# Performance work log

Hardware: AMD Instinct MI355X
Metric: run time of the kernel (lower is better)

The kernel has to match this reference:

```python
import jax, jax.numpy as jnp
import numpy as np

WSZ = 8
HEADS = 8
FILTER_RATE = 0.3
EPS = 1e-5


def layer_norm(x, w, b):
    mu = x.mean(-1, keepdims=True)
    var = ((x - mu) ** 2).mean(-1, keepdims=True)
    return (x - mu) * jax.lax.rsqrt(var + EPS) * w + b


def setup_inputs() -> dict:
    key = jax.random.key(0)
    ks = jax.random.split(key, 8)
    B, C, H, W = 2, 256, 512, 512
    C2 = 2 * C
    s = 0.02
    return {
        "feature_map": jax.random.normal(ks[0], (B, C, H, W), jnp.float32),
        "uncertain_map": jax.random.uniform(ks[1], (B, H, W), jnp.float32),
        "norm_w": jnp.ones((C,), jnp.float32),
        "norm_b": jnp.zeros((C,), jnp.float32),
        "lin0_w": jax.random.normal(ks[2], (C, C2), jnp.float32) * s,
        "lin0_b": jnp.zeros((C2,), jnp.float32),
        "qkv0_w": jax.random.normal(ks[3], (C2, 3 * C2), jnp.float32) * s,
        "lin1_w": jax.random.normal(ks[4], (C2, C2), jnp.float32) * s,
        "lin1_b": jnp.zeros((C2,), jnp.float32),
        "qkv1_w": jax.random.normal(ks[5], (C2, 3 * C2), jnp.float32) * s,
        "proj_w": jax.random.normal(ks[6], (C2, C), jnp.float32) * s,
        "proj_b": jnp.zeros((C,), jnp.float32),
    }


def _window_attn(xf, qkv_w, scale, winsz, C2):
    # xf: (N, winsz, C2)
    qkv = (xf @ qkv_w).reshape(-1, winsz, 3, HEADS, C2 // HEADS)
    q, k, v = qkv[:, :, 0], qkv[:, :, 1], qkv[:, :, 2]  # (N, winsz, H, dh)
    a = jnp.einsum("nqhd,nkhd->nhqk", q, k) * scale
    a = jax.nn.softmax(a, axis=-1)
    o = jnp.einsum("nhqk,nkhd->nqhd", a, v).reshape(-1, winsz, C2)
    return xf + o


def reference(feature_map, uncertain_map, norm_w, norm_b, lin0_w, lin0_b,
              qkv0_w, lin1_w, lin1_b, qkv1_w, proj_w, proj_b):
    B, C, H, W = feature_map.shape
    wsz = WSZ
    nH, nW = H // wsz, W // wsz
    nWin, winsz = nH * nW, wsz * wsz
    nWF = int(nWin * FILTER_RATE)
    C2 = 2 * C
    scale = (C // HEADS) ** -0.5  # module uses C//num_heads, not C2//num_heads

    # window partition
    x = jnp.transpose(feature_map, (0, 2, 3, 1))  # B H W C
    win_x = x.reshape(B, nH, wsz, nW, wsz, C).transpose(0, 1, 3, 2, 4, 5)
    win_x = win_x.reshape(B * nWin, winsz, C)
    win_unc = uncertain_map.reshape(B, nH, wsz, nW, wsz).transpose(0, 1, 3, 2, 4)
    win_unc = win_unc.reshape(B, nWin, winsz)

    # topk window selection by mean uncertainty
    score = win_unc.mean(-1)  # (B, nWin)
    _, idx = jax.lax.top_k(score, nWF)  # (B, nWF)
    flat_idx = (idx + jnp.arange(B)[:, None] * nWin).reshape(-1)  # (B*nWF,)

    xw = win_x[flat_idx]  # gather: (B*nWF, winsz, C)
    xn = layer_norm(xw, norm_w, norm_b)

    # local branch: repeat 0
    xf = jax.nn.gelu(xn @ lin0_w + lin0_b, approximate=False)
    xf = _window_attn(xf, qkv0_w, scale, winsz, C2)
    # repeat 1
    xf = xf + jax.nn.gelu(xf @ lin1_w + lin1_b, approximate=False)
    xf = _window_attn(xf, qkv1_w, scale, winsz, C2)

    out_f = xn + jax.nn.gelu(xf @ proj_w + proj_b, approximate=False)

    # scatter-add back into unnormalized windows
    win_x = win_x.at[flat_idx].add(out_f)

    x = win_x.reshape(B, nH, nW, wsz, wsz, C).transpose(0, 1, 3, 2, 4, 5)
    x = x.reshape(B, H, W, C)
    return jnp.transpose(x, (0, 3, 1, 2))
```

## Files before the change

kernel.cpp:

```cpp
#include <hip/hip_runtime.h>
#include <math.h>

typedef unsigned short u16;
typedef unsigned int   u32;
typedef __attribute__((ext_vector_type(8))) short bf16x8;
typedef __attribute__((ext_vector_type(4))) float f32x4;

#define DEV static __device__ __forceinline__

DEV u16 f2b(float f) {
  union { float f; u32 u; } v; v.f = f;
  u32 r = v.u + 0x7FFFu + ((v.u >> 16) & 1u);
  return (u16)(r >> 16);
}
DEV float b2f(u16 h) {
  union { u32 u; float f; } v; v.u = ((u32)h) << 16;
  return v.f;
}
DEV float gelu_f(float x) { return 0.5f * x * (1.0f + erff(x * 0.70710678118654752f)); }

DEV void gload16(const u16* g, u16* l) {
  __builtin_amdgcn_global_load_lds(
      (const __attribute__((address_space(1))) void*)g,
      (__attribute__((address_space(3))) void*)l, 16, 0, 0);
}

__global__ void k_transpose_w(const float* __restrict__ src, u16* __restrict__ dst,
                              int K, int N) {
  long t = (long)blockIdx.x * 256 + threadIdx.x;
  if (t >= (long)K * N) return;
  int n = (int)(t / K), k = (int)(t % K);
  dst[t] = f2b(src[(long)k * N + n]);
}

__global__ void k_scores(const float* __restrict__ unc, float* __restrict__ scores) {
  int id = blockIdx.x * 256 + threadIdx.x;
  if (id >= 8192) return;
  int b = id >> 12, win = id & 4095;
  int h0 = (win >> 6) << 3, w0 = (win & 63) << 3;
  float r[8] = {0.f,0.f,0.f,0.f,0.f,0.f,0.f,0.f};
  for (int i = 0; i < 8; ++i) {
    long base = ((long)(b * 512 + h0 + i)) * 512 + w0;
    #pragma unroll
    for (int j = 0; j < 8; ++j) r[j] += unc[base + j];
  }
  float s = ((r[0] + r[1]) + (r[2] + r[3])) + ((r[4] + r[5]) + (r[6] + r[7]));
  scores[id] = s * (1.0f / 64.0f);
}

__global__ __launch_bounds__(1024) void k_topk(
    const float* __restrict__ scores, int* __restrict__ row2win,
    int* __restrict__ win2row, int nWF) {
  __shared__ float ls[4096];
  __shared__ int   li[4096];
  const int b = blockIdx.x;
  const int tid = threadIdx.x;
  for (int i = tid; i < 4096; i += 1024) {
    ls[i] = scores[b * 4096 + i];
    li[i] = i;
    win2row[b * 4096 + i] = -1;
  }
  __syncthreads();
  for (int k = 2; k <= 4096; k <<= 1) {
    for (int j = k >> 1; j > 0; j >>= 1) {
      for (int t = tid; t < 2048; t += 1024) {
        int i = ((t / j) * (j << 1)) + (t % j);
        int ixj = i + j;
        bool up = ((i & k) == 0);
        float sa = ls[i], sb = ls[ixj];
        int ia = li[i], ib = li[ixj];
        bool g = (sa > sb) || (sa == sb && ia < ib);
        if (g != up) { ls[i] = sb; ls[ixj] = sa; li[i] = ib; li[ixj] = ia; }
      }
      __syncthreads();
    }
  }
  for (int r = tid; r < nWF; r += 1024) {
    int win = li[r];
    row2win[b * nWF + r] = (b << 12) | win;
    win2row[b * 4096 + win] = b * nWF + r;
  }
}

__global__ __launch_bounds__(256) void k_gather_ln(
    const float* __restrict__ fm, const float* __restrict__ nw,
    const float* __restrict__ nb, const int* __restrict__ row2win,
    u16* __restrict__ xn, int winStart) {
  __shared__ float sx[64 * 256];
  const int tid = threadIdx.x;
  const int rw = row2win[winStart + blockIdx.x];
  const int b = rw >> 12, win = rw & 4095;
  const int h0 = (win >> 6) << 3, w0 = (win & 63) << 3;
  {
    const int c8 = tid >> 3, h = tid & 7;
    #pragma unroll
    for (int cc = 0; cc < 8; ++cc) {
      const int c = cc * 32 + c8;
      long base = ((long)(b * 256 + c) * 512 + h0 + h) * 512 + w0;
      float4 v0 = *(const float4*)(fm + base);
      float4 v1 = *(const float4*)(fm + base + 4);
      float vv[8] = {v0.x, v0.y, v0.z, v0.w, v1.x, v1.y, v1.z, v1.w};
      #pragma unroll
      for (int j = 0; j < 8; ++j) {
        int tok = h * 8 + j;
        sx[tok * 256 + (c ^ ((tok & 15) << 1))] = vv[j];
      }
    }
  }
  __syncthreads();
  const int tok = tid >> 2, g = tid & 3;
  const int swz = (tok & 15) << 1;
  float sum = 0.f;
  for (int q = 0; q < 64; ++q) sum += sx[tok * 256 + ((g * 64 + q) ^ swz)];
  sum += __shfl_xor(sum, 1);
  sum += __shfl_xor(sum, 2);
  const float mu = sum * (1.0f / 256.0f);
  float s2 = 0.f;
  for (int q = 0; q < 64; ++q) {
    float d = sx[tok * 256 + ((g * 64 + q) ^ swz)] - mu;
    s2 += d * d;
  }
  s2 += __shfl_xor(s2, 1);
  s2 += __shfl_xor(s2, 2);
  const float rs = rsqrtf(s2 * (1.0f / 256.0f) + 1e-5f);
  long obase = ((long)blockIdx.x * 64 + tok) * 256 + g * 64;
  for (int q8 = 0; q8 < 8; ++q8) {
    u16 tmp[8];
    #pragma unroll
    for (int e = 0; e < 8; ++e) {
      int c = g * 64 + q8 * 8 + e;
      float v = (sx[tok * 256 + (c ^ swz)] - mu) * rs * nw[c] + nb[c];
      tmp[e] = f2b(v);
    }
    *(ulonglong2*)(xn + obase + q8 * 8) = *(const ulonglong2*)tmp;
  }
}

template <int EPI, int NT, int KD>
__global__ __launch_bounds__(512, 2) void k_gemm256(
    const u16* __restrict__ A, const u16* __restrict__ Bt,
    const float* __restrict__ bias, const u16* __restrict__ Res,
    u16* __restrict__ Y, int N) {
  __shared__ __attribute__((aligned(16))) u16 S[65536];
  const int tid = threadIdx.x;
  const int l = tid & 63, wid = tid >> 6;
  const int wm = wid >> 2, wn = wid & 3;

  const int nwg = gridDim.x;
  const int d = blockIdx.x;
  const int xcd = d & 7, j = d >> 3;
  const int q = nwg >> 3, r8 = nwg & 7;
  const int wrk = (xcd < r8 ? xcd * (q + 1) : r8 * (q + 1) + (xcd - r8) * q) + j;
  const int tm = wrk / NT, tn = wrk % NT;

  const int srow = wid * 8 + (l >> 3);
  const int k0b = ((l & 7) << 4) ^ ((l >> 3) << 4);
  const u16* gA = A + (long)(tm * 256 + srow) * KD + (k0b >> 1);
  const u16* gB = Bt + (long)(tn * 256 + srow) * KD + (k0b >> 1);
  char* ldsS = (char*)S + wid * 1024 + l * 16;
  const char* Sb = (const char*)S;

  f32x4 acc[8][4] = {};
  bf16x8 bfrag[4][2];
  bf16x8 af[2][2];

#define STG(T, ISB, H) do { \
    const u16* g_ = (ISB) ? gB : gA; \
    char* lp_ = ldsS + ((T) & 1) * 65536 + (ISB) * 32768 + (H) * 16384; \
    gload16(g_ + (long)((H) * 128) * KD + (long)(T) * 64, (u16*)lp_); \
    gload16(g_ + (long)((H) * 128 + 64) * KD + (long)(T) * 64, (u16*)(lp_ + 8192)); \
  } while (0)

#define DS_B(T) do { \
    _Pragma("unroll") for (int ni_ = 0; ni_ < 4; ++ni_) { \
      const int r_ = wn * 64 + ni_ * 16 + (l & 15); \
      _Pragma("unroll") for (int kk_ = 0; kk_ < 2; ++kk_) { \
        const int kb_ = kk_ * 64 + ((l >> 4) << 4); \
        bfrag[ni_][kk_] = *(const bf16x8*)(Sb + ((T) & 1) * 65536 + 32768 + r_ * 128 + (kb_ ^ ((r_ & 7) << 4))); \
      } } \
  } while (0)

#define DS_A(T, Q) do { \
    _Pragma("unroll") for (int m2_ = 0; m2_ < 2; ++m2_) { \
      const int r_ = wm * 128 + (2 * (Q) + m2_) * 16 + (l & 15); \
      _Pragma("unroll") for (int kk_ = 0; kk_ < 2; ++kk_) { \
        const int kb_ = kk_ * 64 + ((l >> 4) << 4); \
        af[m2_][kk_] = *(const bf16x8*)(Sb + ((T) & 1) * 65536 + r_ * 128 + (kb_ ^ ((r_ & 7) << 4))); \
      } } \
  } while (0)

#define MFMA16(Q) do { \
    _Pragma("unroll") for (int m2_ = 0; m2_ < 2; ++m2_) \
      _Pragma("unroll") for (int ni_ = 0; ni_ < 4; ++ni_) \
        _Pragma("unroll") for (int kk_ = 0; kk_ < 2; ++kk_) \
          acc[2 * (Q) + m2_][ni_] = __builtin_amdgcn_mfma_f32_16x16x32_bf16( \
              af[m2_][kk_], bfrag[ni_][kk_], acc[2 * (Q) + m2_][ni_], 0, 0, 0); \
  } while (0)

#define BAR_MFMA(Q) do { \
    __builtin_amdgcn_s_barrier(); \
    asm volatile("s_waitcnt lgkmcnt(0)" ::: "memory"); \
    __builtin_amdgcn_sched_barrier(0); \
    __builtin_amdgcn_s_setprio(1); \
    MFMA16(Q); \
    __builtin_amdgcn_s_setprio(0); \
  } while (0)

#define PH_END() do { \
    __builtin_amdgcn_s_barrier(); \
    __builtin_amdgcn_sched_barrier(0); \
  } while (0)

  STG(0, 0, 0); STG(0, 0, 1); STG(0, 1, 0); STG(0, 1, 1);
  STG(1, 0, 0); STG(1, 0, 1); STG(1, 1, 0); STG(1, 1, 1);
  asm volatile("s_waitcnt vmcnt(8)" ::: "memory");
  __builtin_amdgcn_s_barrier();
  __builtin_amdgcn_sched_barrier(0);

  constexpr int nIter = KD >> 7;
  for (int i = 0; i < nIter; ++i) {
    const int t0 = 2 * i, t1 = 2 * i + 1;
    const bool more = (i + 1 < nIter);
    DS_B(t0); DS_A(t0, 0);
    if (i > 0) STG(t1, 0, 0);
    BAR_MFMA(0); PH_END();
    DS_A(t0, 1);
    if (i > 0) STG(t1, 0, 1);
    if (more) STG(t0 + 2, 1, 0);
    BAR_MFMA(1); PH_END();
    DS_A(t0, 2);
    if (more) STG(t0 + 2, 1, 1);
    BAR_MFMA(2); PH_END();
    DS_A(t0, 3);
    BAR_MFMA(3);
    if (more) { asm volatile("s_waitcnt vmcnt(4)" ::: "memory"); }
    else      { asm volatile("s_waitcnt vmcnt(0)" ::: "memory"); }
    PH_END();
    DS_B(t1); DS_A(t1, 0);
    if (more) STG(t0 + 2, 0, 0);
    BAR_MFMA(0); PH_END();
    DS_A(t1, 1);
    if (more) STG(t0 + 2, 0, 1);
    BAR_MFMA(1); PH_END();
    DS_A(t1, 2);
    if (more) STG(t1 + 2, 1, 0);
    BAR_MFMA(2); PH_END();
    DS_A(t1, 3);
    if (more) STG(t1 + 2, 1, 1);
    BAR_MFMA(3);
    if (more) { asm volatile("s_waitcnt vmcnt(4)" ::: "memory"); }
    PH_END();
  }

  if (EPI == 3) {
    float bv[4];
    #pragma unroll
    for (int ni = 0; ni < 4; ++ni)
      bv[ni] = bias[tn * 256 + wn * 64 + ni * 16 + (l & 15)];
    const long rbase = (long)tm * 256 + wm * 128 + ((l >> 4) << 2);
    const int cbase = tn * 256 + wn * 64 + (l & 15);
    #pragma unroll
    for (int mi = 0; mi < 8; ++mi) {
      #pragma unroll
      for (int r = 0; r < 4; ++r) {
        long m = rbase + mi * 16 + r;
        #pragma unroll
        for (int ni = 0; ni < 4; ++ni) {
          int n = cbase + ni * 16;
          float v = gelu_f(acc[mi][ni][r] + bv[ni]);
          v += b2f(Res[m * N + n]);
          Y[((m >> 6) * 256 + n) * 64 + (m & 63)] = f2b(v);
        }
      }
    }
  } else {
    float bv[4];
    if (EPI == 1 || EPI == 2) {
      #pragma unroll
      for (int ni = 0; ni < 4; ++ni)
        bv[ni] = bias[tn * 256 + wn * 64 + ni * 16 + (l & 15)];
    }
    #pragma unroll
    for (int sw = 0; sw < 4; ++sw) {
      #pragma unroll
      for (int mi2 = 0; mi2 < 2; ++mi2) {
        const int mi = 2 * sw + mi2;
        const int lr0 = wm * 32 + mi2 * 16 + ((l >> 4) << 2);
        #pragma unroll
        for (int r = 0; r < 4; ++r) {
          const int lrr = lr0 + r;
          #pragma unroll
          for (int ni = 0; ni < 4; ++ni) {
            float v = acc[mi][ni][r];
            if (EPI == 1 || EPI == 2) v = gelu_f(v + bv[ni]);
            const int col = wn * 64 + ni * 16 + (l & 15);
            S[lrr * 256 + ((((col >> 3) ^ (lrr & 7)) << 3) | (col & 7))] = f2b(v);
          }
        }
      }
      asm volatile("s_waitcnt lgkmcnt(0)" ::: "memory");
      __builtin_amdgcn_s_barrier();
      const int lr2 = tid >> 3;
      const long m = (long)tm * 256 + (lr2 >> 5) * 128 + sw * 32 + (lr2 & 31);
      #pragma unroll
      for (int rd = 0; rd < 4; ++rd) {
        const int chunk = rd * 8 + (tid & 7);
        ulonglong2 val = *(const ulonglong2*)(S + lr2 * 256 + ((chunk ^ (lr2 & 7)) << 3));
        const int n = tn * 256 + chunk * 8;
        if (EPI == 2) {
          u16 tv[8], rv[8];
          *(ulonglong2*)tv = val;
          *(ulonglong2*)rv = *(const ulonglong2*)(Res + m * N + n);
          #pragma unroll
          for (int e = 0; e < 8; ++e) tv[e] = f2b(b2f(tv[e]) + b2f(rv[e]));
          val = *(const ulonglong2*)tv;
        }
        if (EPI == 4) {
          const long win = m >> 6;
          const int t_ = n >> 9, h_ = (n >> 6) & 7, d0 = n & 63;
          *(ulonglong2*)(Y + ((((win * 8 + h_) * 3 + t_) * 64 + (m & 63)) * 64 + d0)) = val;
        } else {
          *(ulonglong2*)(Y + m * N + n) = val;
        }
      }
      if (sw < 3) {
        __builtin_amdgcn_s_barrier();
      }
    }
  }
#undef STG
#undef DS_B
#undef DS_A
#undef MFMA16
#undef BAR_MFMA
#undef PH_END
}

__global__ __launch_bounds__(256) void k_attn(
    const u16* __restrict__ qkv, u16* __restrict__ xf) {
  __shared__ __attribute__((aligned(16))) u16 sq[64 * 64];
  __shared__ __attribute__((aligned(16))) u16 sk[64 * 64];
  __shared__ __attribute__((aligned(16))) u16 sv[64 * 64];
  __shared__ __attribute__((aligned(16))) u16 sp[64 * 64];
  const int tid = threadIdx.x;
  const int l = tid & 63, w = tid >> 6;
  const int wloc = blockIdx.x >> 3, h = blockIdx.x & 7;
  const long tokbase = (long)wloc * 64;
  const u16* base = qkv + (long)blockIdx.x * 12288;

  #pragma unroll
  for (int rd = 0; rd < 6; ++rd) {
    const int cid = rd * 256 + tid;
    ulonglong2 v16 = *(const ulonglong2*)(base + (long)cid * 8);
    const int t = (cid >> 3) & 63, d0 = (cid & 7) << 3;
    if (rd < 2) {
      *(ulonglong2*)((char*)sq + t * 128 + ((d0 * 2) ^ ((t & 7) << 4))) = v16;
    } else if (rd < 4) {
      *(ulonglong2*)((char*)sk + t * 128 + ((d0 * 2) ^ ((t & 7) << 4))) = v16;
    } else {
      u16 vv[8];
      *(ulonglong2*)vv = v16;
      #pragma unroll
      for (int e = 0; e < 8; ++e) {
        int r = d0 + e;
        *(u16*)((char*)sv + r * 128 + ((t * 2) ^ ((r & 7) << 4))) = vv[e];
      }
    }
  }
  __syncthreads();

  f32x4 accs[4] = {};
  #pragma unroll
  for (int ks = 0; ks < 2; ++ks) {
    int kb = ks * 64 + ((l >> 4) << 4);
    int ra = w * 16 + (l & 15);
    bf16x8 aq = *(const bf16x8*)((char*)sq + ra * 128 + (kb ^ ((ra & 7) << 4)));
    #pragma unroll
    for (int cf = 0; cf < 4; ++cf) {
      int rb = cf * 16 + (l & 15);
      bf16x8 bk = *(const bf16x8*)((char*)sk + rb * 128 + (kb ^ ((rb & 7) << 4)));
      accs[cf] = __builtin_amdgcn_mfma_f32_16x16x32_bf16(aq, bk, accs[cf], 0, 0, 0);
    }
  }
  const float scale = 0.17677669529663687f;
  float pv[4][4];
  #pragma unroll
  for (int r = 0; r < 4; ++r) {
    float m = -1e30f;
    #pragma unroll
    for (int cf = 0; cf < 4; ++cf) {
      pv[cf][r] = accs[cf][r] * scale;
      m = fmaxf(m, pv[cf][r]);
    }
    for (int off = 1; off < 16; off <<= 1) m = fmaxf(m, __shfl_xor(m, off));
    float s = 0.f;
    #pragma unroll
    for (int cf = 0; cf < 4; ++cf) { pv[cf][r] = __expf(pv[cf][r] - m); s += pv[cf][r]; }
    for (int off = 1; off < 16; off <<= 1) s += __shfl_xor(s, off);
    float inv = 1.0f / s;
    #pragma unroll
    for (int cf = 0; cf < 4; ++cf) pv[cf][r] *= inv;
  }
  #pragma unroll
  for (int cf = 0; cf < 4; ++cf)
    #pragma unroll
    for (int r = 0; r < 4; ++r) {
      int pr = w * 16 + ((l >> 4) << 2) + r, pc = cf * 16 + (l & 15);
      *(u16*)((char*)sp + pr * 128 + ((pc * 2) ^ ((pr & 7) << 4))) = f2b(pv[cf][r]);
    }
  __syncthreads();

  f32x4 acco[4] = {};
  #pragma unroll
  for (int ks = 0; ks < 2; ++ks) {
    int kb = ks * 64 + ((l >> 4) << 4);
    int ra = w * 16 + (l & 15);
    bf16x8 ap = *(const bf16x8*)((char*)sp + ra * 128 + (kb ^ ((ra & 7) << 4)));
    #pragma unroll
    for (int cf = 0; cf < 4; ++cf) {
      int rb = cf * 16 + (l & 15);
      bf16x8 bvv = *(const bf16x8*)((char*)sv + rb * 128 + (kb ^ ((rb & 7) << 4)));
      acco[cf] = __builtin_amdgcn_mfma_f32_16x16x32_bf16(ap, bvv, acco[cf], 0, 0, 0);
    }
  }
  #pragma unroll
  for (int cf = 0; cf < 4; ++cf)
    #pragma unroll
    for (int r = 0; r < 4; ++r) {
      long m = tokbase + w * 16 + ((l >> 4) << 2) + r;
      int n = h * 64 + cf * 16 + (l & 15);
      long idx = m * 512 + n;
      xf[idx] = f2b(acco[cf][r] + b2f(xf[idx]));
    }
}

__global__ __launch_bounds__(256) void k_assemble(
    const float* __restrict__ fm, const u16* __restrict__ out_f,
    const int* __restrict__ win2row, float* __restrict__ out) {
  const int tid = threadIdx.x;
  const int bq = blockIdx.x;
  const int hw = bq & 63, c = (bq >> 6) & 255, b = bq >> 14;
  const int w0 = (tid & 127) << 2;
  const int hlo = tid >> 7;
  const int win = hw * 64 + (w0 >> 3);
  const int r = win2row[b * 4096 + win];
  const u16* ofb = out_f + ((long)(r < 0 ? 0 : r) * 256 + c) * 64 + (w0 & 7);
  const long base = ((long)(b * 256 + c) * 512 + hw * 8) * 512 + w0;
  #pragma unroll
  for (int jj = 0; jj < 4; ++jj) {
    const int h = jj * 2 + hlo;
    float4 v = *(const float4*)(fm + base + (long)h * 512);
    if (r >= 0) {
      ushort4 ov = *(const ushort4*)(ofb + h * 8);
      v.x += b2f(ov.x);
      v.y += b2f(ov.y);
      v.z += b2f(ov.z);
      v.w += b2f(ov.w);
    }
    *(float4*)(out + base + (long)h * 512) = v;
  }
}

extern "C" void kernel_launch(void* const* d_in, const int* in_sizes, int n_in,
                              void* d_out, int out_size, void* d_ws, size_t ws_size,
                              hipStream_t stream) {
  const float* fm     = (const float*)d_in[0];
  const float* unc    = (const float*)d_in[1];
  const float* nw     = (const float*)d_in[2];
  const float* nb     = (const float*)d_in[3];
  const float* w_lin0 = (const float*)d_in[4];
  const float* b_lin0 = (const float*)d_in[5];
  const float* w_qkv0 = (const float*)d_in[6];
  const float* w_lin1 = (const float*)d_in[7];
  const float* b_lin1 = (const float*)d_in[8];
  const float* w_qkv1 = (const float*)d_in[9];
  const float* w_proj = (const float*)d_in[10];
  const float* b_proj = (const float*)d_in[11];
  float* out = (float*)d_out;

  const int nWF = 1228, totWin = 2456;
  const long totTok = (long)totWin * 64;

  char* p = (char*)d_ws;
  auto alloc = [&](size_t bytes) {
    char* r = p;
    p += (bytes + 255) & ~(size_t)255;
    return r;
  };
  float* scores = (float*)alloc(8192 * 4);
  int* win2row  = (int*)alloc(8192 * 4);
  int* row2win  = (int*)alloc(totWin * 4);
  u16* wT       = (u16*)alloc((size_t)2097152 * 2);
  u16* out_f    = (u16*)alloc((size_t)(totTok + 256) * 256 * 2);
  size_t persist = (size_t)(p - (char*)d_ws);

  int wpc = totWin;
  {
    const int cands[6] = {1, 2, 4, 8, 16, 32};
    for (int ci = 0; ci < 6; ++ci) {
      int n = cands[ci];
      int wp = ((totWin + n - 1) / n + 3) & ~3;
      size_t mc = (size_t)wp * 64;
      size_t need = persist + 4096 +
                    ((mc * 256 * 2 + 255) & ~(size_t)255) +
                    2 * ((mc * 512 * 2 + 255) & ~(size_t)255) +
                    ((mc * 1536 * 2 + 255) & ~(size_t)255);
      if (need <= ws_size) { wpc = wp; break; }
    }
  }
  long mcap = (long)wpc * 64;
  u16* xn   = (u16*)alloc((size_t)mcap * 256 * 2);
  u16* xfa  = (u16*)alloc((size_t)mcap * 512 * 2);
  u16* xfb  = (u16*)alloc((size_t)mcap * 512 * 2);
  u16* qkvb = (u16*)alloc((size_t)mcap * 1536 * 2);

  u16* wT_lin0 = wT;
  u16* wT_qkv0 = wT + 131072;
  u16* wT_lin1 = wT + 917504;
  u16* wT_qkv1 = wT + 1179648;
  u16* wT_proj = wT + 1966080;
  k_transpose_w<<<(131072 + 255) / 256, 256, 0, stream>>>(w_lin0, wT_lin0, 256, 512);
  k_transpose_w<<<(786432 + 255) / 256, 256, 0, stream>>>(w_qkv0, wT_qkv0, 512, 1536);
  k_transpose_w<<<(262144 + 255) / 256, 256, 0, stream>>>(w_lin1, wT_lin1, 512, 512);
  k_transpose_w<<<(786432 + 255) / 256, 256, 0, stream>>>(w_qkv1, wT_qkv1, 512, 1536);
  k_transpose_w<<<(131072 + 255) / 256, 256, 0, stream>>>(w_proj, wT_proj, 512, 256);

  k_scores<<<32, 256, 0, stream>>>(unc, scores);
  k_topk<<<2, 1024, 0, stream>>>(scores, row2win, win2row, nWF);

  for (int w0 = 0; w0 < totWin; w0 += wpc) {
    int rem = totWin - w0;
    int wn = (wpc < rem) ? wpc : rem;
    int mT = wn / 4;
    k_gather_ln<<<wn, 256, 0, stream>>>(fm, nw, nb, row2win, xn, w0);
    k_gemm256<1, 2, 256><<<mT * 2, 512, 0, stream>>>(xn, wT_lin0, b_lin0, nullptr, xfa, 512);
    k_gemm256<4, 6, 512><<<mT * 6, 512, 0, stream>>>(xfa, wT_qkv0, nullptr, nullptr, qkvb, 1536);
    k_attn<<<wn * 8, 256, 0, stream>>>(qkvb, xfa);
    k_gemm256<2, 2, 512><<<mT * 2, 512, 0, stream>>>(xfa, wT_lin1, b_lin1, xfa, xfb, 512);
    k_gemm256<4, 6, 512><<<mT * 6, 512, 0, stream>>>(xfb, wT_qkv1, nullptr, nullptr, qkvb, 1536);
    k_attn<<<wn * 8, 256, 0, stream>>>(qkvb, xfb);
    k_gemm256<3, 1, 512><<<mT * 1, 512, 0, stream>>>(xfb, wT_proj, b_proj, xn,
                                                     out_f + (long)w0 * 16384, 256);
  }
  k_assemble<<<32768, 256, 0, stream>>>(fm, out_f, win2row, out);
}
```

Baseline: 1.902 ms.

## Stage GEMM and attention epilogues through LDS for vectorized coalesced stores

The GEMM epilogue for the proj/residual path now writes gelu outputs into a swizzled LDS tile, then reads them back so each thread handles 8 contiguous tokens. Those threads emit 16-byte transposed stores into the window-major output. The attention output residual add gets the same treatment: results are staged in LDS and added to xf with 16-byte vector loads and stores instead of scattered 2-byte accesses. This aims to cut uncoalesced global traffic, at the cost of an extra barrier and LDS round trip. The residual reads in the GEMM epilogue remain strided per element, and the extra bf16 rounding before the residual add changes numerics slightly.

Measured after the change: 1.759 ms (median of 2 runs). -7.5%, faster.

```diff
diff --git a/kernel.cpp b/kernel.cpp
--- a/kernel.cpp
+++ b/kernel.cpp
@@ -257,21 +257,34 @@
     #pragma unroll
     for (int ni = 0; ni < 4; ++ni)
       bv[ni] = bias[tn * 256 + wn * 64 + ni * 16 + (l & 15)];
-    const long rbase = (long)tm * 256 + wm * 128 + ((l >> 4) << 2);
-    const int cbase = tn * 256 + wn * 64 + (l & 15);
     #pragma unroll
     for (int mi = 0; mi < 8; ++mi) {
       #pragma unroll
       for (int r = 0; r < 4; ++r) {
-        long m = rbase + mi * 16 + r;
+        const int ml = wm * 128 + mi * 16 + ((l >> 4) << 2) + r;
         #pragma unroll
         for (int ni = 0; ni < 4; ++ni) {
-          int n = cbase + ni * 16;
+          const int nl = wn * 64 + ni * 16 + (l & 15);
           float v = gelu_f(acc[mi][ni][r] + bv[ni]);
-          v += b2f(Res[m * N + n]);
-          Y[((m >> 6) * 256 + n) * 64 + (m & 63)] = f2b(v);
+          S[nl * 256 + ((((ml >> 3) ^ ((nl & 7) << 2)) << 3) | (ml & 7))] = f2b(v);
         }
       }
+    }
+    asm volatile("s_waitcnt lgkmcnt(0)" ::: "memory");
+    __builtin_amdgcn_s_barrier();
+    #pragma unroll
+    for (int rd = 0; rd < 16; ++rd) {
+      const int id = rd * 512 + tid;
+      const int nl = id >> 5, c8 = id & 31;
+      ulonglong2 val = *(const ulonglong2*)(S + nl * 256 + ((c8 ^ ((nl & 7) << 2)) << 3));
+      u16 tv[8];
+      *(ulonglong2*)tv = val;
+      const long mg = (long)tm * 256 + c8 * 8;
+      const int ng = tn * 256 + nl;
+      #pragma unroll
+      for (int e = 0; e < 8; ++e) tv[e] = f2b(b2f(tv[e]) + b2f(Res[(mg + e) * N + ng]));
+      const long row = (mg >> 6);
+      *(ulonglong2*)(Y + (row * 256 + ng) * 64 + (c8 & 7) * 8) = *(const ulonglong2*)tv;
     }
   } else {
     float bv[4];
@@ -427,11 +440,26 @@
   for (int cf = 0; cf < 4; ++cf)
     #pragma unroll
     for (int r = 0; r < 4; ++r) {
-      long m = tokbase + w * 16 + ((l >> 4) << 2) + r;
-      int n = h * 64 + cf * 16 + (l & 15);
-      long idx = m * 512 + n;
-      xf[idx] = f2b(acco[cf][r] + b2f(xf[idx]));
-    }
+      int orow = w * 16 + ((l >> 4) << 2) + r, ocol = cf * 16 + (l & 15);
+      *(u16*)((char*)sq + orow * 128 + ((ocol * 2) ^ ((orow & 7) << 4))) = f2b(acco[cf][r]);
+    }
+  __syncthreads();
+  {
+    const int row = tid >> 2, c32 = tid & 3;
+    const long gaddr = (tokbase + row) * 512 + h * 64 + c32 * 16;
+    #pragma unroll
+    for (int hh = 0; hh < 2; ++hh) {
+      const int colb = c32 * 32 + hh * 16;
+      ulonglong2 ov = *(const ulonglong2*)((char*)sq + row * 128 + (colb ^ ((row & 7) << 4)));
+      ulonglong2 xv = *(const ulonglong2*)(xf + gaddr + hh * 8);
+      u16 o16[8], x16[8];
+      *(ulonglong2*)o16 = ov;
+      *(ulonglong2*)x16 = xv;
+      #pragma unroll
+      for (int e = 0; e < 8; ++e) x16[e] = f2b(b2f(x16[e]) + b2f(o16[e]));
+      *(ulonglong2*)(xf + gaddr + hh * 8) = *(const ulonglong2*)x16;
+    }
+  }
 }
 
 __global__ __launch_bounds__(256) void k_assemble(
```
